# Kernel tuning notes

Measured on AMD Instinct MI355X. Metric: run time of the kernel, lower is better.

The kernel has to match this reference:

```python
import jax, jax.numpy as jnp
import numpy as np

# Static network configuration (from the cfg json in the original module)
BPL = [1, 1536, 1536, 1536, 1536]            # buckets per layer; layer 0 must be 1 (original code indexes inflows[0] only)
L = len(BPL)
NSPIG = [BPL[l + 1] if l < L - 1 else 1 for l in range(L)]  # spigots per bucket in each layer
MAX_B = max(BPL)
MAX_S = max(NSPIG)
G = 9.81
T = 4                                         # number of update_network timesteps


def _spigot_mask():
    # mask[l, b, s] = 1 if bucket b and spigot s exist in layer l (matches the zero-padding in initialize_theta_values)
    m = np.zeros((L, MAX_B, MAX_S), np.float32)
    for l in range(L):
        m[l, :BPL[l], :NSPIG[l]] = 1.0
    return jnp.asarray(m)


def _solve_layer(H0b, sp_h_l, sp_a_l, th_l):
    """Vectorized solve_single_bucket across all buckets of one layer.
    H0b: [B] head after adding inflow. sp_h_l/sp_a_l/th_l: [B, S].
    Sequential over spigots: H_effective = H0b - cumsum(flows)/2.
    Returns (H_new [B], s_q [B, S])."""
    def step(cum, x):
        hh, aa, tt = x                         # each [B]
        h = jnp.maximum(0.0, H0b - 0.5 * cum - hh)
        # safe sqrt (same forward value; avoids nan grad at h == 0)
        v = tt * jnp.sqrt(2.0 * G * jnp.where(h > 0, h, 1.0))
        flow = jnp.where(h > 0, v * aa, 0.0)
        return cum + flow, flow

    xs = (sp_h_l.T, sp_a_l.T, th_l.T)          # [S, B]
    Q, flows = jax.lax.scan(step, jnp.zeros_like(H0b), xs)
    return H0b - Q, flows.T                    # H = (H + inflow) - sum(s_q)


def setup_inputs() -> dict:
    key = jax.random.key(0)
    k1, k2, k3, k4 = jax.random.split(key, 4)
    theta = jax.random.uniform(k1, (L, MAX_B, MAX_S), jnp.float32)   # padded theta table
    sp_h = jax.random.uniform(k2, (L, MAX_B, MAX_S), jnp.float32)    # spigot heights
    sp_a = jax.random.uniform(k3, (L, MAX_B, MAX_S), jnp.float32)    # spigot areas
    H_init = jnp.ones((L, MAX_B), jnp.float32)                        # initial_head_in_buckets = 1.0
    precip = jax.random.uniform(k4, (T,), jnp.float32)                # precip per update step
    return {"theta": theta, "sp_h": sp_h, "sp_a": sp_a, "H_init": H_init, "precip": precip}


def reference(theta, sp_h, sp_a, H_init, precip):
    mask = _spigot_mask()
    theta_m = theta * mask                     # zero theta on padded buckets/spigots -> zero flows there

    def step_t(H_all, p):
        ppl = p / L                            # precip_inflow_per_layer
        H_new = []
        sq_prev = None
        for l in range(L):
            if l == 0:
                inflow = jnp.zeros((MAX_B,), H_all.dtype).at[0].set(ppl)
            else:
                # inflow[j] = sum over upstream buckets of s_q[i, j] + ppl / n_buckets
                inflow = sq_prev.sum(axis=0) + ppl / BPL[l]
            Hn, sq = _solve_layer(H_all[l] + inflow, sp_h[l], sp_a[l], theta_m[l])
            H_new.append(Hn)
            sq_prev = sq
        # network_outflow = sum of last layer s_q
        return jnp.stack(H_new), sq_prev.sum()

    _, outflows = jax.lax.scan(step_t, H_init, precip)
    return outflows                            # [T] network outflow per update step
```

## Files before the change

kernel.cpp:

```cpp
#include <hip/hip_runtime.h>

#define NB 1536
#define NS 1536
#define TSTEPS 4
#define KC  4.4294469180704688f
#define HKC 2.2147234590352344f

#define OFF_KHT 0ull
#define OFF_KH0 (OFF_KHT + 3ull * NS * NB * 8)
#define OFF_KH4 (OFF_KH0 + (unsigned long long)NS * 8)
#define OFF_H   (OFF_KH4 + (unsigned long long)NB * 8)
#define OFF_FB0 (OFF_H + 5ull * NB * 4)
#define OFF_PART (OFF_FB0 + 2ull * NS * 4)

static __device__ __forceinline__ float asqrt(float x) { return __builtin_amdgcn_sqrtf(x); }

#define SS0(HK, HY, F)                      \
  {                                         \
    float e_ = fmaxf(R - (HY), 0.0f);       \
    float q_ = asqrt(e_);                   \
    R = fmaf(-(HK), q_, R);                 \
    F = (HK)*q_;                            \
  }

#define SST(HK, HY, SL)                     \
  {                                         \
    float e_ = fmaxf(R - (HY), 0.0f);       \
    float q_ = asqrt(e_);                   \
    R = fmaf(-(HK), q_, R);                 \
    red[SL][lane] = (HK)*q_;                \
  }

#define LB(P0,P1,P2,P3,P4,P5,P6,P7, sp)                           \
  { const float2* q_ = kh + (size_t)(sp) * NB;                    \
    P0 = q_[0];            P1 = q_[(size_t)NB];                   \
    P2 = q_[2*(size_t)NB]; P3 = q_[3*(size_t)NB];                 \
    P4 = q_[4*(size_t)NB]; P5 = q_[5*(size_t)NB];                 \
    P6 = q_[6*(size_t)NB]; P7 = q_[7*(size_t)NB]; }

#define CB(P0,P1,P2,P3,P4,P5,P6,P7, SL)                           \
  { SST(P0.x,P0.y,(SL)+0) SST(P1.x,P1.y,(SL)+1)                   \
    SST(P2.x,P2.y,(SL)+2) SST(P3.x,P3.y,(SL)+3)                   \
    SST(P4.x,P4.y,(SL)+4) SST(P5.x,P5.y,(SL)+5)                   \
    SST(P6.x,P6.y,(SL)+6) SST(P7.x,P7.y,(SL)+7) }

static __device__ void scan0_lds(const float4* __restrict__ k0, float* __restrict__ fbrow,
                                 float* __restrict__ H0, float P) {
  float R = P;
  float4 c0 = k0[0], c1 = k0[1], c2 = k0[2], c3 = k0[3];
  float4 n0 = k0[4], n1 = k0[5], n2 = k0[6], n3 = k0[7];
#pragma unroll 1
  for (int g = 0; g < NS / 8; ++g) {
    int mi = (g + 2 < NS / 8) ? 4 * g + 8 : 0;
    float4 m0 = k0[mi], m1 = k0[mi + 1], m2 = k0[mi + 2], m3 = k0[mi + 3];
    float f0, f1, f2, f3, f4, f5, f6, f7;
    SS0(c0.x, c0.y, f0) SS0(c0.z, c0.w, f1)
    SS0(c1.x, c1.y, f2) SS0(c1.z, c1.w, f3)
    SS0(c2.x, c2.y, f4) SS0(c2.z, c2.w, f5)
    SS0(c3.x, c3.y, f6) SS0(c3.z, c3.w, f7)
    ((float4*)fbrow)[2 * g]     = make_float4(f0, f1, f2, f3);
    ((float4*)fbrow)[2 * g + 1] = make_float4(f4, f5, f6, f7);
    c0 = n0; c1 = n1; c2 = n2; c3 = n3;
    n0 = m0; n1 = m1; n2 = m2; n3 = m3;
  }
  *H0 = 2.0f * R - P;
}

__global__ __launch_bounds__(256) void prep_k(const float* __restrict__ th,
                                              const float* __restrict__ hh,
                                              const float* __restrict__ aa,
                                              const float* __restrict__ Hinit,
                                              float2* __restrict__ kh0,
                                              float2* __restrict__ kh4,
                                              float* __restrict__ H,
                                              float* __restrict__ out) {
  int i = blockIdx.x * 256 + threadIdx.x;
  if (i < NS) {
    kh0[i] = make_float2(th[i] * aa[i] * HKC, hh[i]);
    size_t i4 = ((size_t)4 * NB + i) * NS;
    kh4[i] = make_float2(th[i4] * aa[i4] * KC, hh[i4]);
  }
  if (i < 5 * NB && i != 0) H[i] = Hinit[i];
  if (i < TSTEPS) out[i] = 0.0f;
}

__global__ __launch_bounds__(256) void transpose_k(const float* __restrict__ th,
                                                   const float* __restrict__ hh,
                                                   const float* __restrict__ aa,
                                                   float2* __restrict__ khT,
                                                   const float2* __restrict__ kh0,
                                                   const float* __restrict__ Hinit,
                                                   const float* __restrict__ precip,
                                                   float* __restrict__ H,
                                                   float* __restrict__ fb0) {
  __shared__ float2 tile[64][65];
  __shared__ float4 k0lds[NS / 2];
  if (blockIdx.z == 3) {
    if (blockIdx.x || blockIdx.y) return;
    int lane = threadIdx.x;
    for (int i = lane; i < NS / 2; i += 256) k0lds[i] = ((const float4*)kh0)[i];
    __syncthreads();
    if (lane) return;
    scan0_lds(k0lds, fb0 , H, Hinit[0] + precip[0] * 0.2f);
    return;
  }
  int l = blockIdx.z + 1;
  int b0 = blockIdx.x * 64, s0 = blockIdx.y * 64;
  int lane = threadIdx.x & 63, ty = threadIdx.x >> 6;
  size_t base = (size_t)l * NB * NS;
#pragma unroll
  for (int r = 0; r < 64; r += 4) {
    int b = b0 + r + ty;
    size_t idx = base + (size_t)b * NS + s0 + lane;
    tile[r + ty][lane] = make_float2(th[idx] * aa[idx] * HKC, hh[idx]);
  }
  __syncthreads();
#pragma unroll
  for (int r = 0; r < 64; r += 4) {
    int s = s0 + r + ty;
    khT[((size_t)blockIdx.z * NS + s) * NB + b0 + lane] = tile[lane][r + ty];
  }
}

__global__ __launch_bounds__(64) void stage_k(
    const float2* __restrict__ khT, const float2* __restrict__ kh0,
    const float2* __restrict__ kh4, float* __restrict__ H,
    float* __restrict__ fb0, float* __restrict__ part,
    const float* __restrict__ precip, float* __restrict__ out, int d) {
  __shared__ float red[64][64];
  __shared__ float4 k0lds[NS / 2];
  int blk = blockIdx.x;
  int lane = threadIdx.x;

  if (blk == 96) {
    int t = d;
    if (t >= TSTEPS) return;
    for (int i = lane; i < NS / 2; i += 64) k0lds[i] = ((const float4*)kh0)[i];
    __syncthreads();
    if (lane) return;
    scan0_lds(k0lds, fb0 + (size_t)(t & 1) * NS, H, H[0] + precip[t] * 0.2f);
    return;
  }
  int track = blk / 24, b = blk % 24;
  int l = track + 1;
  int t = d - l;
  if (t < 0 || t >= TSTEPS) return;
  int par = t & 1;
  float ppl = precip[t] * 0.2f;
  int j = b * 64 + lane;

  if (l == 4) {
    const float* pr = part + ((size_t)(2 * 2 + par) * 24) * NS + j;
    float s_ = 0.f;
#pragma unroll
    for (int i = 0; i < 24; ++i) s_ += pr[(size_t)i * NS];
    float P = H[4 * NB + j] + 2.0f * s_ + ppl * (1.0f / NB);
    float2 kh = kh4[j];
    float e = fmaxf(P - kh.y, 0.0f);
    float fl = kh.x * asqrt(e);
    H[4 * NB + j] = P - fl;
    for (int o = 32; o; o >>= 1) fl += __shfl_xor(fl, o);
    if (lane == 0) atomicAdd(out + t, fl);
    return;
  }

  float inf;
  if (l == 1) {
    inf = 2.0f * fb0[(size_t)par * NS + j];
  } else {
    const float* pr = part + ((size_t)((l - 2) * 2 + par) * 24) * NS + j;
    float s_ = 0.f;
#pragma unroll
    for (int i = 0; i < 24; ++i) s_ += pr[(size_t)i * NS];
    inf = 2.0f * s_;
  }
  float P = H[l * NB + j] + inf + ppl * (1.0f / NB);
  float R = P;
  const float2* kh = khT + (size_t)(l - 1) * NS * NB + j;
  float* part_row = part + ((size_t)((l - 1) * 2 + par) * 24 + b) * NS;

  float2 A0,A1,A2,A3,A4,A5,A6,A7, B0,B1,B2,B3,B4,B5,B6,B7;
  float2 C0,C1,C2,C3,C4,C5,C6,C7, D0,D1,D2,D3,D4,D5,D6,D7;
  float2 E0,E1,E2,E3,E4,E5,E6,E7, F0,F1,F2,F3,F4,F5,F6,F7;
  float2 G0,G1,G2,G3,G4,G5,G6,G7, X0,X1,X2,X3,X4,X5,X6,X7;
  LB(A0,A1,A2,A3,A4,A5,A6,A7, 0)
  LB(B0,B1,B2,B3,B4,B5,B6,B7, 8)
  LB(C0,C1,C2,C3,C4,C5,C6,C7, 16)
  LB(D0,D1,D2,D3,D4,D5,D6,D7, 24)
  LB(E0,E1,E2,E3,E4,E5,E6,E7, 32)
  LB(F0,F1,F2,F3,F4,F5,F6,F7, 40)
  LB(G0,G1,G2,G3,G4,G5,G6,G7, 48)
  LB(X0,X1,X2,X3,X4,X5,X6,X7, 56)
#pragma unroll 1
  for (int s = 0; s < NS; s += 64) {
    int sA = (s + 64 < NS) ? s + 64 : 0;
    int sE = (s + 96 < NS) ? s + 96 : 0;
    CB(A0,A1,A2,A3,A4,A5,A6,A7, 0)   LB(A0,A1,A2,A3,A4,A5,A6,A7, sA)
    CB(B0,B1,B2,B3,B4,B5,B6,B7, 8)   LB(B0,B1,B2,B3,B4,B5,B6,B7, sA + 8)
    CB(C0,C1,C2,C3,C4,C5,C6,C7, 16)  LB(C0,C1,C2,C3,C4,C5,C6,C7, sA + 16)
    CB(D0,D1,D2,D3,D4,D5,D6,D7, 24)  LB(D0,D1,D2,D3,D4,D5,D6,D7, sA + 24)
    CB(E0,E1,E2,E3,E4,E5,E6,E7, 32)  LB(E0,E1,E2,E3,E4,E5,E6,E7, sE)
    CB(F0,F1,F2,F3,F4,F5,F6,F7, 40)  LB(F0,F1,F2,F3,F4,F5,F6,F7, sE + 8)
    CB(G0,G1,G2,G3,G4,G5,G6,G7, 48)  LB(G0,G1,G2,G3,G4,G5,G6,G7, sE + 16)
    CB(X0,X1,X2,X3,X4,X5,X6,X7, 56)  LB(X0,X1,X2,X3,X4,X5,X6,X7, sE + 24)
    {
      const float4* rowq = (const float4*)&red[lane][0];
      float a0 = 0.f, a1 = 0.f, a2 = 0.f, a3 = 0.f;
#pragma unroll
      for (int c = 0; c < 16; ++c) {
        float4 v = rowq[(c + lane) & 15];
        a0 += v.x; a1 += v.y; a2 += v.z; a3 += v.w;
      }
      part_row[s + lane] = (a0 + a1) + (a2 + a3);
    }
  }
  H[l * NB + j] = 2.0f * R - P;
}

extern "C" void kernel_launch(void* const* d_in, const int* in_sizes, int n_in,
                              void* d_out, int out_size, void* d_ws,
                              size_t ws_size, hipStream_t stream) {
  const float* theta = (const float*)d_in[0];
  const float* sp_h = (const float*)d_in[1];
  const float* sp_a = (const float*)d_in[2];
  const float* Hinit = (const float*)d_in[3];
  const float* precip = (const float*)d_in[4];
  float* out = (float*)d_out;

  char* ws = (char*)d_ws;
  float2* khT = (float2*)(ws + OFF_KHT);
  float2* kh0 = (float2*)(ws + OFF_KH0);
  float2* kh4 = (float2*)(ws + OFF_KH4);
  float* H = (float*)(ws + OFF_H);
  float* fb0 = (float*)(ws + OFF_FB0);
  float* part = (float*)(ws + OFF_PART);

  hipLaunchKernelGGL(prep_k, dim3(30), dim3(256), 0, stream, theta, sp_h, sp_a,
                     Hinit, kh0, kh4, H, out);
  hipLaunchKernelGGL(transpose_k, dim3(24, 24, 4), dim3(256), 0, stream, theta,
                     sp_h, sp_a, khT, kh0, Hinit, precip, H, fb0);
  for (int d = 1; d < TSTEPS + 4; ++d) {
    hipLaunchKernelGGL(stage_k, dim3(97), dim3(64), 0, stream, khT, kh0, kh4, H,
                       fb0, part, precip, out, d);
  }
}
```

Measured before the change: 467.2 us.

## Fuse transpose into stage kernel with producer wave filling LDS tiles

Removes the separate transpose kernel and its khT workspace. Each stage block now has a producer wave that streams theta/area/height directly from the raw inputs into a double-buffered LDS tile and also does the partial-sum reductions. The consumer wave runs the sequential spigot scan reading from LDS. Stage kernels are templated on the step index. This trades the one-off transpose pass for re-reading raw inputs at every timestep and for a block barrier per chunk.

```diff
diff --git a/kernel.cpp b/kernel.cpp
--- a/kernel.cpp
+++ b/kernel.cpp
@@ -5,44 +5,23 @@
 #define TSTEPS 4
 #define KC  4.4294469180704688f
 #define HKC 2.2147234590352344f
-
-#define OFF_KHT 0ull
-#define OFF_KH0 (OFF_KHT + 3ull * NS * NB * 8)
-#define OFF_KH4 (OFF_KH0 + (unsigned long long)NS * 8)
+#define CHUNK 32
+#define NCH (NS / CHUNK)
+
+#define OFF_KH4 0ull
 #define OFF_H   (OFF_KH4 + (unsigned long long)NB * 8)
 #define OFF_FB0 (OFF_H + 5ull * NB * 4)
 #define OFF_PART (OFF_FB0 + 2ull * NS * 4)
 
 static __device__ __forceinline__ float asqrt(float x) { return __builtin_amdgcn_sqrtf(x); }
 
-#define SS0(HK, HY, F)                      \
+#define SST(HK, HY, DST)                    \
   {                                         \
     float e_ = fmaxf(R - (HY), 0.0f);       \
     float q_ = asqrt(e_);                   \
     R = fmaf(-(HK), q_, R);                 \
-    F = (HK)*q_;                            \
-  }
-
-#define SST(HK, HY, SL)                     \
-  {                                         \
-    float e_ = fmaxf(R - (HY), 0.0f);       \
-    float q_ = asqrt(e_);                   \
-    R = fmaf(-(HK), q_, R);                 \
-    red[SL][lane] = (HK)*q_;                \
-  }
-
-#define LB(P0,P1,P2,P3,P4,P5,P6,P7, sp)                           \
-  { const float2* q_ = kh + (size_t)(sp) * NB;                    \
-    P0 = q_[0];            P1 = q_[(size_t)NB];                   \
-    P2 = q_[2*(size_t)NB]; P3 = q_[3*(size_t)NB];                 \
-    P4 = q_[4*(size_t)NB]; P5 = q_[5*(size_t)NB];                 \
-    P6 = q_[6*(size_t)NB]; P7 = q_[7*(size_t)NB]; }
-
-#define CB(P0,P1,P2,P3,P4,P5,P6,P7, SL)                           \
-  { SST(P0.x,P0.y,(SL)+0) SST(P1.x,P1.y,(SL)+1)                   \
-    SST(P2.x,P2.y,(SL)+2) SST(P3.x,P3.y,(SL)+3)                   \
-    SST(P4.x,P4.y,(SL)+4) SST(P5.x,P5.y,(SL)+5)                   \
-    SST(P6.x,P6.y,(SL)+6) SST(P7.x,P7.y,(SL)+7) }
+    DST = (HK)*q_;                          \
+  }
 
 static __device__ void scan0_lds(const float4* __restrict__ k0, float* __restrict__ fbrow,
                                  float* __restrict__ H0, float P) {
@@ -54,10 +33,10 @@
     int mi = (g + 2 < NS / 8) ? 4 * g + 8 : 0;
     float4 m0 = k0[mi], m1 = k0[mi + 1], m2 = k0[mi + 2], m3 = k0[mi + 3];
     float f0, f1, f2, f3, f4, f5, f6, f7;
-    SS0(c0.x, c0.y, f0) SS0(c0.z, c0.w, f1)
-    SS0(c1.x, c1.y, f2) SS0(c1.z, c1.w, f3)
-    SS0(c2.x, c2.y, f4) SS0(c2.z, c2.w, f5)
-    SS0(c3.x, c3.y, f6) SS0(c3.z, c3.w, f7)
+    SST(c0.x, c0.y, f0) SST(c0.z, c0.w, f1)
+    SST(c1.x, c1.y, f2) SST(c1.z, c1.w, f3)
+    SST(c2.x, c2.y, f4) SST(c2.z, c2.w, f5)
+    SST(c3.x, c3.y, f6) SST(c3.z, c3.w, f7)
     ((float4*)fbrow)[2 * g]     = make_float4(f0, f1, f2, f3);
     ((float4*)fbrow)[2 * g + 1] = make_float4(f4, f5, f6, f7);
     c0 = n0; c1 = n1; c2 = n2; c3 = n3;
@@ -66,17 +45,32 @@
   *H0 = 2.0f * R - P;
 }
 
+static __device__ void fuse_k0(const float* __restrict__ th, const float* __restrict__ hh,
+                               const float* __restrict__ aa, float2* __restrict__ k0t,
+                               int tid, int nthr) {
+  for (int s = tid; s < NS; s += nthr)
+    k0t[s] = make_float2(th[s] * aa[s] * HKC, hh[s]);
+}
+
 __global__ __launch_bounds__(256) void prep_k(const float* __restrict__ th,
                                               const float* __restrict__ hh,
                                               const float* __restrict__ aa,
                                               const float* __restrict__ Hinit,
-                                              float2* __restrict__ kh0,
+                                              const float* __restrict__ precip,
                                               float2* __restrict__ kh4,
                                               float* __restrict__ H,
+                                              float* __restrict__ fb0,
                                               float* __restrict__ out) {
+  __shared__ float4 k0t4[NS / 2];
+  if (blockIdx.x == 30) {
+    fuse_k0(th, hh, aa, (float2*)k0t4, threadIdx.x, 256);
+    __syncthreads();
+    if (threadIdx.x) return;
+    scan0_lds(k0t4, fb0 , H, Hinit[0] + precip[0] * 0.2f);
+    return;
+  }
   int i = blockIdx.x * 256 + threadIdx.x;
   if (i < NS) {
-    kh0[i] = make_float2(th[i] * aa[i] * HKC, hh[i]);
     size_t i4 = ((size_t)4 * NB + i) * NS;
     kh4[i] = make_float2(th[i4] * aa[i4] * KC, hh[i4]);
   }
@@ -84,73 +78,39 @@
   if (i < TSTEPS) out[i] = 0.0f;
 }
 
-__global__ __launch_bounds__(256) void transpose_k(const float* __restrict__ th,
-                                                   const float* __restrict__ hh,
-                                                   const float* __restrict__ aa,
-                                                   float2* __restrict__ khT,
-                                                   const float2* __restrict__ kh0,
-                                                   const float* __restrict__ Hinit,
-                                                   const float* __restrict__ precip,
-                                                   float* __restrict__ H,
-                                                   float* __restrict__ fb0) {
-  __shared__ float2 tile[64][65];
-  __shared__ float4 k0lds[NS / 2];
-  if (blockIdx.z == 3) {
-    if (blockIdx.x || blockIdx.y) return;
-    int lane = threadIdx.x;
-    for (int i = lane; i < NS / 2; i += 256) k0lds[i] = ((const float4*)kh0)[i];
-    __syncthreads();
-    if (lane) return;
-    scan0_lds(k0lds, fb0 , H, Hinit[0] + precip[0] * 0.2f);
+template <int D>
+__global__ __launch_bounds__(128) void stage_k(
+    const float* __restrict__ th, const float* __restrict__ hh,
+    const float* __restrict__ aa, const float2* __restrict__ kh4,
+    float* __restrict__ H, float* __restrict__ fb0, float* __restrict__ part,
+    const float* __restrict__ precip, float* __restrict__ out) {
+  __shared__ float2 ptile[2][CHUNK][66];
+  __shared__ float red[2][CHUNK][64];
+  __shared__ float4 k0t4[NS / 2];
+  int blk = blockIdx.x;
+  int tid = threadIdx.x;
+  int lane = tid & 63, wv = tid >> 6;
+
+  if (blk == 96) {
+    constexpr int t = D;
+    if (t >= TSTEPS) return;
+    fuse_k0(th, hh, aa, (float2*)k0t4, tid, 128);
+    __syncthreads();
+    if (tid) return;
+    scan0_lds(k0t4, fb0 + (size_t)(t & 1) * NS, H, H[0] + precip[t] * 0.2f);
     return;
   }
-  int l = blockIdx.z + 1;
-  int b0 = blockIdx.x * 64, s0 = blockIdx.y * 64;
-  int lane = threadIdx.x & 63, ty = threadIdx.x >> 6;
-  size_t base = (size_t)l * NB * NS;
-#pragma unroll
-  for (int r = 0; r < 64; r += 4) {
-    int b = b0 + r + ty;
-    size_t idx = base + (size_t)b * NS + s0 + lane;
-    tile[r + ty][lane] = make_float2(th[idx] * aa[idx] * HKC, hh[idx]);
-  }
-  __syncthreads();
-#pragma unroll
-  for (int r = 0; r < 64; r += 4) {
-    int s = s0 + r + ty;
-    khT[((size_t)blockIdx.z * NS + s) * NB + b0 + lane] = tile[lane][r + ty];
-  }
-}
-
-__global__ __launch_bounds__(64) void stage_k(
-    const float2* __restrict__ khT, const float2* __restrict__ kh0,
-    const float2* __restrict__ kh4, float* __restrict__ H,
-    float* __restrict__ fb0, float* __restrict__ part,
-    const float* __restrict__ precip, float* __restrict__ out, int d) {
-  __shared__ float red[64][64];
-  __shared__ float4 k0lds[NS / 2];
-  int blk = blockIdx.x;
-  int lane = threadIdx.x;
-
-  if (blk == 96) {
-    int t = d;
-    if (t >= TSTEPS) return;
-    for (int i = lane; i < NS / 2; i += 64) k0lds[i] = ((const float4*)kh0)[i];
-    __syncthreads();
-    if (lane) return;
-    scan0_lds(k0lds, fb0 + (size_t)(t & 1) * NS, H, H[0] + precip[t] * 0.2f);
-    return;
-  }
   int track = blk / 24, b = blk % 24;
-  int l = track + 1;
-  int t = d - l;
+  const int l = track + 1;
+  const int t = D - l;
   if (t < 0 || t >= TSTEPS) return;
-  int par = t & 1;
+  const int par = t & 1;
   float ppl = precip[t] * 0.2f;
   int j = b * 64 + lane;
 
   if (l == 4) {
-    const float* pr = part + ((size_t)(2 * 2 + par) * 24) * NS + j;
+    if (wv) return;
+    const float* pr = part + ((size_t)(4 + par) * 24) * NS + j;
     float s_ = 0.f;
 #pragma unroll
     for (int i = 0; i < 24; ++i) s_ += pr[(size_t)i * NS];
@@ -164,57 +124,96 @@
     return;
   }
 
-  float inf;
-  if (l == 1) {
-    inf = 2.0f * fb0[(size_t)par * NS + j];
+  size_t pbase = (size_t)l * NB * NS + (size_t)(b * 64) * NS;
+  float* part_row = part + ((size_t)((l - 1) * 2 + par) * 24 + b) * NS;
+
+  if (wv == 0) {
+    float inf;
+    if (l == 1) {
+      inf = 2.0f * fb0[(size_t)par * NS + j];
+    } else {
+      const float* pr = part + ((size_t)((l - 2) * 2 + par) * 24) * NS + j;
+      float s_ = 0.f;
+#pragma unroll
+      for (int i = 0; i < 24; ++i) s_ += pr[(size_t)i * NS];
+      inf = 2.0f * s_;
+    }
+    float P = H[(size_t)l * NB + j] + inf + ppl * (1.0f / NB);
+    float R = P;
+#define LD8(Q0,Q1,Q2,Q3,Q4,Q5,Q6,Q7, BUF, G)            \
+    { const float2* pt_ = &ptile[BUF][(G) * 8][0];      \
+      Q0 = pt_[0 * 66 + lane]; Q1 = pt_[1 * 66 + lane]; \
+      Q2 = pt_[2 * 66 + lane]; Q3 = pt_[3 * 66 + lane]; \
+      Q4 = pt_[4 * 66 + lane]; Q5 = pt_[5 * 66 + lane]; \
+      Q6 = pt_[6 * 66 + lane]; Q7 = pt_[7 * 66 + lane]; }
+#define CN8(Q0,Q1,Q2,Q3,Q4,Q5,Q6,Q7, BUF, G)                       \
+    { float* rr_ = &red[BUF][(G) * 8][0];                          \
+      SST(Q0.x, Q0.y, rr_[0 * 64 + lane])                          \
+      SST(Q1.x, Q1.y, rr_[1 * 64 + lane])                          \
+      SST(Q2.x, Q2.y, rr_[2 * 64 + lane])                          \
+      SST(Q3.x, Q3.y, rr_[3 * 64 + lane])                          \
+      SST(Q4.x, Q4.y, rr_[4 * 64 + lane])                          \
+      SST(Q5.x, Q5.y, rr_[5 * 64 + lane])                          \
+      SST(Q6.x, Q6.y, rr_[6 * 64 + lane])                          \
+      SST(Q7.x, Q7.y, rr_[7 * 64 + lane]) }
+#pragma unroll 1
+    for (int c = 0; c < NCH; ++c) {
+      __syncthreads();
+      int bf = c & 1;
+      float2 X0,X1,X2,X3,X4,X5,X6,X7, Y0,Y1,Y2,Y3,Y4,Y5,Y6,Y7;
+      LD8(X0,X1,X2,X3,X4,X5,X6,X7, bf, 0)
+      LD8(Y0,Y1,Y2,Y3,Y4,Y5,Y6,Y7, bf, 1)
+      CN8(X0,X1,X2,X3,X4,X5,X6,X7, bf, 0)
+      LD8(X0,X1,X2,X3,X4,X5,X6,X7, bf, 2)
+      CN8(Y0,Y1,Y2,Y3,Y4,Y5,Y6,Y7, bf, 1)
+      LD8(Y0,Y1,Y2,Y3,Y4,Y5,Y6,Y7, bf, 3)
+      CN8(X0,X1,X2,X3,X4,X5,X6,X7, bf, 2)
+      CN8(Y0,Y1,Y2,Y3,Y4,Y5,Y6,Y7, bf, 3)
+    }
+    __syncthreads();
+    H[(size_t)l * NB + j] = 2.0f * R - P;
   } else {
-    const float* pr = part + ((size_t)((l - 2) * 2 + par) * 24) * NS + j;
-    float s_ = 0.f;
-#pragma unroll
-    for (int i = 0; i < 24; ++i) s_ += pr[(size_t)i * NS];
-    inf = 2.0f * s_;
-  }
-  float P = H[l * NB + j] + inf + ppl * (1.0f / NB);
-  float R = P;
-  const float2* kh = khT + (size_t)(l - 1) * NS * NB + j;
-  float* part_row = part + ((size_t)((l - 1) * 2 + par) * 24 + b) * NS;
-
-  float2 A0,A1,A2,A3,A4,A5,A6,A7, B0,B1,B2,B3,B4,B5,B6,B7;
-  float2 C0,C1,C2,C3,C4,C5,C6,C7, D0,D1,D2,D3,D4,D5,D6,D7;
-  float2 E0,E1,E2,E3,E4,E5,E6,E7, F0,F1,F2,F3,F4,F5,F6,F7;
-  float2 G0,G1,G2,G3,G4,G5,G6,G7, X0,X1,X2,X3,X4,X5,X6,X7;
-  LB(A0,A1,A2,A3,A4,A5,A6,A7, 0)
-  LB(B0,B1,B2,B3,B4,B5,B6,B7, 8)
-  LB(C0,C1,C2,C3,C4,C5,C6,C7, 16)
-  LB(D0,D1,D2,D3,D4,D5,D6,D7, 24)
-  LB(E0,E1,E2,E3,E4,E5,E6,E7, 32)
-  LB(F0,F1,F2,F3,F4,F5,F6,F7, 40)
-  LB(G0,G1,G2,G3,G4,G5,G6,G7, 48)
-  LB(X0,X1,X2,X3,X4,X5,X6,X7, 56)
+    int fr = lane >> 3, fs4 = lane & 7;
+#define FILL(BUF, CC)                                                        \
+    { int s0_ = (CC) * CHUNK;                                                \
+      _Pragma("unroll")                                                      \
+      for (int k = 0; k < 8; ++k) {                                          \
+        int r_ = fr + 8 * k;                                                 \
+        size_t gi_ = pbase + (size_t)r_ * NS + s0_ + fs4 * 4;                \
+        float4 t4_ = *(const float4*)(th + gi_);                             \
+        float4 a4_ = *(const float4*)(aa + gi_);                             \
+        float4 h4_ = *(const float4*)(hh + gi_);                             \
+        float2* pt_ = &ptile[BUF][fs4 * 4][r_];                              \
+        pt_[0 * 66] = make_float2(t4_.x * a4_.x * HKC, h4_.x);               \
+        pt_[1 * 66] = make_float2(t4_.y * a4_.y * HKC, h4_.y);               \
+        pt_[2 * 66] = make_float2(t4_.z * a4_.z * HKC, h4_.z);               \
+        pt_[3 * 66] = make_float2(t4_.w * a4_.w * HKC, h4_.w);               \
+      } }
+    FILL(0, 0)
+    int rs = lane & 31, rh = lane >> 5;
 #pragma unroll 1
-  for (int s = 0; s < NS; s += 64) {
-    int sA = (s + 64 < NS) ? s + 64 : 0;
-    int sE = (s + 96 < NS) ? s + 96 : 0;
-    CB(A0,A1,A2,A3,A4,A5,A6,A7, 0)   LB(A0,A1,A2,A3,A4,A5,A6,A7, sA)
-    CB(B0,B1,B2,B3,B4,B5,B6,B7, 8)   LB(B0,B1,B2,B3,B4,B5,B6,B7, sA + 8)
-    CB(C0,C1,C2,C3,C4,C5,C6,C7, 16)  LB(C0,C1,C2,C3,C4,C5,C6,C7, sA + 16)
-    CB(D0,D1,D2,D3,D4,D5,D6,D7, 24)  LB(D0,D1,D2,D3,D4,D5,D6,D7, sA + 24)
-    CB(E0,E1,E2,E3,E4,E5,E6,E7, 32)  LB(E0,E1,E2,E3,E4,E5,E6,E7, sE)
-    CB(F0,F1,F2,F3,F4,F5,F6,F7, 40)  LB(F0,F1,F2,F3,F4,F5,F6,F7, sE + 8)
-    CB(G0,G1,G2,G3,G4,G5,G6,G7, 48)  LB(G0,G1,G2,G3,G4,G5,G6,G7, sE + 16)
-    CB(X0,X1,X2,X3,X4,X5,X6,X7, 56)  LB(X0,X1,X2,X3,X4,X5,X6,X7, sE + 24)
+    for (int c = 0; c < NCH; ++c) {
+      __syncthreads();
+      if (c + 1 < NCH) FILL((c + 1) & 1, c + 1)
+      if (c >= 1) {
+        const float* rr = &red[(c - 1) & 1][rs][0];
+        float acc = 0.f;
+#pragma unroll
+        for (int i = 0; i < 32; ++i) acc += rr[((i + lane) & 31) + rh * 32];
+        acc += __shfl_xor(acc, 32);
+        if (rh == 0) part_row[(c - 1) * CHUNK + rs] = acc;
+      }
+    }
+    __syncthreads();
     {
-      const float4* rowq = (const float4*)&red[lane][0];
-      float a0 = 0.f, a1 = 0.f, a2 = 0.f, a3 = 0.f;
-#pragma unroll
-      for (int c = 0; c < 16; ++c) {
-        float4 v = rowq[(c + lane) & 15];
-        a0 += v.x; a1 += v.y; a2 += v.z; a3 += v.w;
-      }
-      part_row[s + lane] = (a0 + a1) + (a2 + a3);
-    }
-  }
-  H[l * NB + j] = 2.0f * R - P;
+      const float* rr = &red[(NCH - 1) & 1][rs][0];
+      float acc = 0.f;
+#pragma unroll
+      for (int i = 0; i < 32; ++i) acc += rr[((i + lane) & 31) + rh * 32];
+      acc += __shfl_xor(acc, 32);
+      if (rh == 0) part_row[(NCH - 1) * CHUNK + rs] = acc;
+    }
+  }
 }
 
 extern "C" void kernel_launch(void* const* d_in, const int* in_sizes, int n_in,
@@ -228,19 +227,21 @@
   float* out = (float*)d_out;
 
   char* ws = (char*)d_ws;
-  float2* khT = (float2*)(ws + OFF_KHT);
-  float2* kh0 = (float2*)(ws + OFF_KH0);
   float2* kh4 = (float2*)(ws + OFF_KH4);
   float* H = (float*)(ws + OFF_H);
   float* fb0 = (float*)(ws + OFF_FB0);
   float* part = (float*)(ws + OFF_PART);
 
-  hipLaunchKernelGGL(prep_k, dim3(30), dim3(256), 0, stream, theta, sp_h, sp_a,
-                     Hinit, kh0, kh4, H, out);
-  hipLaunchKernelGGL(transpose_k, dim3(24, 24, 4), dim3(256), 0, stream, theta,
-                     sp_h, sp_a, khT, kh0, Hinit, precip, H, fb0);
-  for (int d = 1; d < TSTEPS + 4; ++d) {
-    hipLaunchKernelGGL(stage_k, dim3(97), dim3(64), 0, stream, khT, kh0, kh4, H,
-                       fb0, part, precip, out, d);
-  }
-}
+  hipLaunchKernelGGL(prep_k, dim3(31), dim3(256), 0, stream, theta, sp_h, sp_a,
+                     Hinit, precip, kh4, H, fb0, out);
+#define LAUNCH_STAGE(DD)                                                       \
+  hipLaunchKernelGGL(HIP_KERNEL_NAME(stage_k<DD>), dim3(97), dim3(128), 0,     \
+                     stream, theta, sp_h, sp_a, kh4, H, fb0, part, precip, out)
+  LAUNCH_STAGE(1);
+  LAUNCH_STAGE(2);
+  LAUNCH_STAGE(3);
+  LAUNCH_STAGE(4);
+  LAUNCH_STAGE(5);
+  LAUNCH_STAGE(6);
+  LAUNCH_STAGE(7);
+}
```

After: 535.1 us. 14.5% more time.
